# Optimization experiments

Hardware: AMD Instinct MI355X
Metric: run time of the kernel (lower is better)

Reference implementation:

```python
import jax, jax.numpy as jnp
import numpy as np

DETECTIONS_PER_IMG = 36
NMS_THRESH = 0.5
SCORE_THRESH = 0.2
MIN_SIZE = 0.01
NMS_TOPK = 2048  # fixed candidate budget for jit-compatible NMS
BBOX_XFORM_CLIP = float(np.log(1000.0 / 16.0))
WX, WY, WW, WH = 10.0, 10.0, 5.0, 5.0  # torchvision BoxCoder weights


def _decode(reg, props):
    # reg: [N, C*4], props: [N, 4] -> decoded boxes [N, C, 4] (torchvision BoxCoder.decode)
    widths = props[:, 2] - props[:, 0]
    heights = props[:, 3] - props[:, 1]
    ctr_x = props[:, 0] + 0.5 * widths
    ctr_y = props[:, 1] + 0.5 * heights
    reg = reg.reshape(reg.shape[0], -1, 4)
    dx = reg[..., 0] / WX
    dy = reg[..., 1] / WY
    dw = jnp.minimum(reg[..., 2] / WW, BBOX_XFORM_CLIP)
    dh = jnp.minimum(reg[..., 3] / WH, BBOX_XFORM_CLIP)
    pcx = dx * widths[:, None] + ctr_x[:, None]
    pcy = dy * heights[:, None] + ctr_y[:, None]
    pw = jnp.exp(dw) * widths[:, None]
    ph = jnp.exp(dh) * heights[:, None]
    return jnp.stack([pcx - 0.5 * pw, pcy - 0.5 * ph,
                      pcx + 0.5 * pw, pcy + 0.5 * ph], axis=-1)


def _pairwise_iou(boxes):
    # boxes: [K, 4] -> IoU [K, K]
    area = (boxes[:, 2] - boxes[:, 0]) * (boxes[:, 3] - boxes[:, 1])
    lt = jnp.maximum(boxes[:, None, :2], boxes[None, :, :2])
    rb = jnp.minimum(boxes[:, None, 2:], boxes[None, :, 2:])
    wh = jnp.clip(rb - lt, 0.0)
    inter = wh[..., 0] * wh[..., 1]
    union = area[:, None] + area[None, :] - inter
    return jnp.where(union > 0, inter / union, 0.0)


def _per_image(logits, reg, props, feats, img_hw):
    # logits [N, C], reg [N, C*4], props [N, 4], feats [N, D], img_hw [2] (h, w)
    N, C = logits.shape
    boxes = _decode(reg, props)[:, 1:, :].reshape(-1, 4)     # drop background, [N*(C-1), 4]
    scores = jax.nn.softmax(logits, axis=-1)[:, 1:].reshape(-1)
    h = img_hw[0].astype(boxes.dtype)
    w = img_hw[1].astype(boxes.dtype)
    x1 = jnp.clip(boxes[:, 0], 0.0, w)
    y1 = jnp.clip(boxes[:, 1], 0.0, h)
    x2 = jnp.clip(boxes[:, 2], 0.0, w)
    y2 = jnp.clip(boxes[:, 3], 0.0, h)
    boxes = jnp.stack([x1, y1, x2, y2], axis=-1)
    # score threshold + remove_small_boxes as a validity mask
    valid = (scores > SCORE_THRESH) & ((x2 - x1) >= MIN_SIZE) & ((y2 - y1) >= MIN_SIZE)
    masked = jnp.where(valid, scores, -jnp.inf)
    top_s, top_i = jax.lax.top_k(masked, NMS_TOPK)          # candidates in score order
    tboxes = boxes[top_i]
    tvalid = jnp.isfinite(top_s)
    iou = _pairwise_iou(tboxes)                              # [K, K]
    ar = jnp.arange(NMS_TOPK)

    def body(i, keep):
        sup = keep[i] & (iou[i] > NMS_THRESH) & (ar > i)
        return keep & ~sup

    keep = jax.lax.fori_loop(0, NMS_TOPK, body, tvalid)
    # first DETECTIONS_PER_IMG kept candidates, in score order (stable sort: kept first)
    order = jnp.argsort(jnp.where(keep, 0, 1), stable=True)[:DETECTIONS_PER_IMG]
    sel_keep = keep[order]
    prop_idx = top_i[order] // (C - 1)                       # candidate -> proposal row
    out = feats[prop_idx] * sel_keep[:, None].astype(feats.dtype)  # zero-pad missing slots
    return out


def setup_inputs() -> dict:
    key = jax.random.key(0)
    k0, k1, k2, k3, k4 = jax.random.split(key, 5)
    B, N, C, D = 8, 1000, 91, 1024
    class_logits = jax.random.normal(k0, (B, N, C), dtype=jnp.float32) * 3.0
    box_regression = jax.random.normal(k1, (B, N, C * 4), dtype=jnp.float32) * 0.5
    xy = jax.random.uniform(k2, (B, N, 2), minval=0.0, maxval=700.0)
    wh = jax.random.uniform(k3, (B, N, 2), minval=20.0, maxval=100.0)
    proposals = jnp.concatenate([xy, xy + wh], axis=-1).astype(jnp.float32)
    box_features = jax.random.normal(k4, (B, N, D), dtype=jnp.float32)
    image_shapes = jnp.full((B, 2), 800, dtype=jnp.int32)
    return {"class_logits": class_logits, "box_regression": box_regression,
            "proposals": proposals, "box_features": box_features,
            "image_shapes": image_shapes}


def reference(class_logits, box_regression, proposals, box_features, image_shapes):
    # returns [B, DETECTIONS_PER_IMG, D]
    return jax.vmap(_per_image)(class_logits, box_regression, proposals,
                                box_features, image_shapes)
```

## Files before the change

### kernel.cpp

```cpp
#include <hip/hip_runtime.h>
#include <stdint.h>

#define B 8
#define N 1000
#define C 91
#define NC 90
#define D 1024
#define KMAX 2048
#define PAD 4096
#define DETS 36
#define SCORE_THRESH 0.2f
#define NMS_THRESH 0.5f
#define MIN_SIZE 0.01f
#define XFORM_CLIP 4.135166556742356f

__device__ __forceinline__ void decode_clip(const float* __restrict__ rg,
                                            float wdt, float hgt, float cx, float cy,
                                            float W, float H,
                                            float& x1, float& y1, float& x2, float& y2) {
    float dx = rg[0] / 10.0f;
    float dy = rg[1] / 10.0f;
    float dw = fminf(rg[2] / 5.0f, XFORM_CLIP);
    float dh = fminf(rg[3] / 5.0f, XFORM_CLIP);
    float pcx = dx * wdt + cx;
    float pcy = dy * hgt + cy;
    float pw  = expf(dw) * wdt;
    float ph  = expf(dh) * hgt;
    x1 = fminf(fmaxf(pcx - 0.5f * pw, 0.0f), W);
    y1 = fminf(fmaxf(pcy - 0.5f * ph, 0.0f), H);
    x2 = fminf(fmaxf(pcx + 0.5f * pw, 0.0f), W);
    y2 = fminf(fmaxf(pcy + 0.5f * ph, 0.0f), H);
}

__global__ __launch_bounds__(256) void k_score(const float* __restrict__ logits,
                        const float* __restrict__ reg,
                        const float* __restrict__ props,
                        const int* __restrict__ img_hw,
                        unsigned long long* __restrict__ keys) {
    int b = blockIdx.x / 250;
    int local = blockIdx.x % 250;
    int wib = threadIdx.x >> 6, lane = threadIdx.x & 63;
    int n = local * 4 + wib;
    int r = b * N + n;

    __shared__ unsigned long long slot[4][4];
    if (threadIdx.x < 16) slot[threadIdx.x >> 2][threadIdx.x & 3] = 0ULL;
    __syncthreads();

    const float* lg = logits + (size_t)r * C;
    float v0 = lg[lane];
    float v1 = (lane < C - 64) ? lg[64 + lane] : -3.4e38f;
    float m = fmaxf(v0, v1);
    #pragma unroll
    for (int off = 32; off; off >>= 1) m = fmaxf(m, __shfl_xor(m, off, 64));
    float e0 = expf(v0 - m);
    float e1 = (lane < C - 64) ? expf(v1 - m) : 0.0f;
    float s = e0 + e1;
    #pragma unroll
    for (int off = 32; off; off >>= 1) s += __shfl_xor(s, off, 64);

    float p0 = props[r * 4 + 0], p1 = props[r * 4 + 1];
    float p2 = props[r * 4 + 2], p3 = props[r * 4 + 3];
    float wdt = p2 - p0, hgt = p3 - p1;
    float cx = p0 + 0.5f * wdt, cy = p1 + 0.5f * hgt;
    float H = (float)img_hw[b * 2 + 0];
    float W = (float)img_hw[b * 2 + 1];

    unsigned long long keyv[2] = {0ULL, 0ULL};
    #pragma unroll
    for (int t2 = 0; t2 < 2; ++t2) {
        int c = lane + t2 * 64;
        float e = t2 ? e1 : e0;
        if (c >= 1 && c < C) {
            float sc = e / s;
            if (sc > SCORE_THRESH) {
                const float* rg = reg + (size_t)r * (C * 4) + (size_t)c * 4;
                float x1, y1, x2, y2;
                decode_clip(rg, wdt, hgt, cx, cy, W, H, x1, y1, x2, y2);
                if ((x2 - x1) >= MIN_SIZE && (y2 - y1) >= MIN_SIZE) {
                    unsigned int idx = (unsigned int)(n * NC + (c - 1));
                    keyv[t2] = ((unsigned long long)__float_as_uint(sc) << 32) |
                               (unsigned long long)(0xFFFFFFFFu - idx);
                }
            }
        }
    }
    unsigned long long m0 = __ballot(keyv[0] != 0ULL);
    unsigned long long m1 = __ballot(keyv[1] != 0ULL);
    unsigned long long lower = (1ULL << lane) - 1ULL;
    if (keyv[0]) slot[wib][__popcll(m0 & lower)] = keyv[0];
    if (keyv[1]) slot[wib][__popcll(m0) + __popcll(m1 & lower)] = keyv[1];
    __syncthreads();
    if (threadIdx.x < 16) {
        int ww = threadIdx.x >> 2, p = threadIdx.x & 3;
        keys[(size_t)b * PAD + (size_t)(local * 4 + ww) * 4 + p] = slot[ww][p];
    }
}

__global__ __launch_bounds__(256) void k_rank(int* __restrict__ Kvals,
                                              const unsigned long long* __restrict__ keys,
                                              const float* __restrict__ reg,
                                              const float* __restrict__ props,
                                              const int* __restrict__ img_hw,
                                              float* __restrict__ bx1, float* __restrict__ by1,
                                              float* __restrict__ bx2, float* __restrict__ by2,
                                              int* __restrict__ propn) {
    __shared__ unsigned long long sk[PAD];
    __shared__ int pc[256];
    int b = blockIdx.y;
    const unsigned long long* kb = keys + (size_t)b * PAD;
    for (int t = threadIdx.x; t < PAD; t += 256)
        sk[t] = (t < 4 * N) ? kb[t] : 0ULL;
    __syncthreads();

    int rloc = threadIdx.x & 63;
    int quarter = threadIdx.x >> 6;
    int row = blockIdx.x * 64 + rloc;
    unsigned long long my = sk[row];
    int base = quarter * 1024;
    int cnt = 0;
    #pragma unroll 8
    for (int it = 0; it < 1024; ++it)
        cnt += (sk[base + it] > my) ? 1 : 0;
    pc[threadIdx.x] = cnt;
    __syncthreads();

    if (quarter == 0) {
        int rank = pc[rloc] + pc[rloc + 64] + pc[rloc + 128] + pc[rloc + 192];
        if (row == 4 * N) Kvals[b] = (rank < KMAX) ? rank : KMAX;
        if (my != 0ULL && rank < KMAX) {
            unsigned int idx = 0xFFFFFFFFu - (unsigned int)(my & 0xFFFFFFFFull);
            int n = (int)(idx / NC);
            int c = (int)(idx % NC) + 1;
            int r = b * N + n;
            float p0 = props[r * 4 + 0], p1 = props[r * 4 + 1];
            float p2 = props[r * 4 + 2], p3 = props[r * 4 + 3];
            float wdt = p2 - p0, hgt = p3 - p1;
            float cx = p0 + 0.5f * wdt, cy = p1 + 0.5f * hgt;
            float H = (float)img_hw[b * 2 + 0];
            float W = (float)img_hw[b * 2 + 1];
            const float* rg = reg + (size_t)r * (C * 4) + (size_t)c * 4;
            float x1, y1, x2, y2;
            decode_clip(rg, wdt, hgt, cx, cy, W, H, x1, y1, x2, y2);
            size_t o = (size_t)b * KMAX + rank;
            bx1[o] = x1; by1[o] = y1; bx2[o] = x2; by2[o] = y2;
            propn[o] = n;
        }
    }
}

__global__ __launch_bounds__(64) void k_nms(const int* __restrict__ Kvals,
                                            const float* __restrict__ bx1, const float* __restrict__ by1,
                                            const float* __restrict__ bx2, const float* __restrict__ by2,
                                            const int* __restrict__ propn,
                                            int* __restrict__ sel) {
    __shared__ float kx1[DETS], ky1[DETS], kx2[DETS], ky2[DETS];
    __shared__ int kpn[DETS];
    int b = blockIdx.x, lane = threadIdx.x;
    int K = Kvals[b];
    size_t ofs = (size_t)b * KMAX;
    int kept = 0;

    for (int cs = 0; cs < K && kept < DETS; cs += 64) {
        int j = cs + lane;
        bool inr = (j < K);
        int jj = inr ? j : 0;
        float x1 = bx1[ofs + jj], y1 = by1[ofs + jj];
        float x2 = bx2[ofs + jj], y2 = by2[ofs + jj];
        int pn = propn[ofs + jj];
        float area = (x2 - x1) * (y2 - y1);

        bool supp = !inr;
        for (int k = 0; k < kept; ++k) {
            float c1 = kx1[k], c2 = ky1[k], c3 = kx2[k], c4 = ky2[k];
            float carea = (c3 - c1) * (c4 - c2);
            float ix1 = fmaxf(c1, x1), iy1 = fmaxf(c2, y1);
            float ix2 = fminf(c3, x2), iy2 = fminf(c4, y2);
            float iw = fmaxf(ix2 - ix1, 0.0f), ih = fmaxf(iy2 - iy1, 0.0f);
            float inter = iw * ih;
            float uni = carea + area - inter;
            float iou = (uni > 0.0f) ? (inter / uni) : 0.0f;
            supp = supp || (iou > NMS_THRESH);
        }
        unsigned long long live = __ballot(!supp);
        while (live != 0ULL && kept < DETS) {
            int i = __ffsll((unsigned long long)live) - 1;
            float c1 = __shfl(x1, i, 64), c2 = __shfl(y1, i, 64);
            float c3 = __shfl(x2, i, 64), c4 = __shfl(y2, i, 64);
            int   cp = __shfl(pn, i, 64);
            if (lane == 0) { kx1[kept] = c1; ky1[kept] = c2; kx2[kept] = c3; ky2[kept] = c4; kpn[kept] = cp; }
            kept++;
            float carea = (c3 - c1) * (c4 - c2);
            float ix1 = fmaxf(c1, x1), iy1 = fmaxf(c2, y1);
            float ix2 = fminf(c3, x2), iy2 = fminf(c4, y2);
            float iw = fmaxf(ix2 - ix1, 0.0f), ih = fmaxf(iy2 - iy1, 0.0f);
            float inter = iw * ih;
            float uni = carea + area - inter;
            float iou = (uni > 0.0f) ? (inter / uni) : 0.0f;
            live &= ~__ballot(iou > NMS_THRESH);
        }
    }
    __syncthreads();
    if (lane < DETS) sel[b * DETS + lane] = (lane < kept) ? kpn[lane] : -1;
}

__global__ __launch_bounds__(256) void k_gather(const int* __restrict__ sel,
                                                const float* __restrict__ feats,
                                                float* __restrict__ out) {
    int slot = blockIdx.x;
    int b = slot / DETS;
    int row = sel[slot];
    float4* o = (float4*)(out + (size_t)slot * D);
    if (row >= 0) {
        const float4* f = (const float4*)(feats + ((size_t)b * N + row) * D);
        o[threadIdx.x] = f[threadIdx.x];
    } else {
        o[threadIdx.x] = make_float4(0.f, 0.f, 0.f, 0.f);
    }
}

extern "C" void kernel_launch(void* const* d_in, const int* in_sizes, int n_in,
                              void* d_out, int out_size, void* d_ws, size_t ws_size,
                              hipStream_t stream) {
    const float* logits = (const float*)d_in[0];
    const float* reg    = (const float*)d_in[1];
    const float* props  = (const float*)d_in[2];
    const float* feats  = (const float*)d_in[3];
    const int*   img    = (const int*)d_in[4];
    float* out = (float*)d_out;

    char* ws = (char*)d_ws;
    int* Kvals    = (int*)(ws + 0);
    int* sel      = (int*)(ws + 256);
    unsigned long long* keys = (unsigned long long*)(ws + 4096);
    float* bx1 = (float*)(ws + 270336);
    float* by1 = (float*)(ws + 335872);
    float* bx2 = (float*)(ws + 401408);
    float* by2 = (float*)(ws + 466944);
    int*   propn = (int*)(ws + 532480);

    k_score<<<dim3(B * 250), dim3(256), 0, stream>>>(logits, reg, props, img, keys);
    k_rank<<<dim3(64, B), dim3(256), 0, stream>>>(Kvals, keys,
        reg, props, img, bx1, by1, bx2, by2, propn);
    k_nms<<<dim3(B), dim3(64), 0, stream>>>(Kvals, bx1, by1, bx2, by2, propn, sel);
    k_gather<<<dim3(B * DETS), dim3(256), 0, stream>>>(sel, feats, out);
}
```

Measured before the change: 122.0 us.

## Register-block rank counting and fuse NMS with feature gather

Result: slower. 131.4 us (+7.7%).

```diff
diff --git a/kernel.cpp b/kernel.cpp
--- a/kernel.cpp
+++ b/kernel.cpp
@@ -97,7 +97,7 @@
     }
 }
 
-__global__ __launch_bounds__(256) void k_rank(int* __restrict__ Kvals,
+__global__ __launch_bounds__(512) void k_rank(int* __restrict__ Kvals,
                                               const unsigned long long* __restrict__ keys,
                                               const float* __restrict__ reg,
                                               const float* __restrict__ props,
@@ -106,27 +106,43 @@
                                               float* __restrict__ bx2, float* __restrict__ by2,
                                               int* __restrict__ propn) {
     __shared__ unsigned long long sk[PAD];
-    __shared__ int pc[256];
+    __shared__ int partial[8][256];
     int b = blockIdx.y;
     const unsigned long long* kb = keys + (size_t)b * PAD;
-    for (int t = threadIdx.x; t < PAD; t += 256)
+    for (int t = threadIdx.x; t < PAD; t += 512)
         sk[t] = (t < 4 * N) ? kb[t] : 0ULL;
     __syncthreads();
 
-    int rloc = threadIdx.x & 63;
-    int quarter = threadIdx.x >> 6;
-    int row = blockIdx.x * 64 + rloc;
-    unsigned long long my = sk[row];
-    int base = quarter * 1024;
-    int cnt = 0;
+    int w = threadIdx.x >> 6;
+    int lane = threadIdx.x & 63;
+    int rbase = blockIdx.x * 256;
+    unsigned long long my0 = sk[rbase + lane];
+    unsigned long long my1 = sk[rbase + lane + 64];
+    unsigned long long my2 = sk[rbase + lane + 128];
+    unsigned long long my3 = sk[rbase + lane + 192];
+    int c0 = 0, c1 = 0, c2 = 0, c3 = 0;
+    int base = w * 512;
     #pragma unroll 8
-    for (int it = 0; it < 1024; ++it)
-        cnt += (sk[base + it] > my) ? 1 : 0;
-    pc[threadIdx.x] = cnt;
-    __syncthreads();
-
-    if (quarter == 0) {
-        int rank = pc[rloc] + pc[rloc + 64] + pc[rloc + 128] + pc[rloc + 192];
+    for (int it = 0; it < 512; ++it) {
+        unsigned long long k = sk[base + it];
+        c0 += (k > my0) ? 1 : 0;
+        c1 += (k > my1) ? 1 : 0;
+        c2 += (k > my2) ? 1 : 0;
+        c3 += (k > my3) ? 1 : 0;
+    }
+    partial[w][lane]       = c0;
+    partial[w][lane + 64]  = c1;
+    partial[w][lane + 128] = c2;
+    partial[w][lane + 192] = c3;
+    __syncthreads();
+
+    if (threadIdx.x < 256) {
+        int rl = threadIdx.x;
+        int rank = 0;
+        #pragma unroll
+        for (int q = 0; q < 8; ++q) rank += partial[q][rl];
+        int row = rbase + rl;
+        unsigned long long my = sk[row];
         if (row == 4 * N) Kvals[b] = (rank < KMAX) ? rank : KMAX;
         if (my != 0ULL && rank < KMAX) {
             unsigned int idx = 0xFFFFFFFFu - (unsigned int)(my & 0xFFFFFFFFull);
@@ -149,73 +165,72 @@
     }
 }
 
-__global__ __launch_bounds__(64) void k_nms(const int* __restrict__ Kvals,
-                                            const float* __restrict__ bx1, const float* __restrict__ by1,
-                                            const float* __restrict__ bx2, const float* __restrict__ by2,
-                                            const int* __restrict__ propn,
-                                            int* __restrict__ sel) {
+__global__ __launch_bounds__(256) void k_nmsg(const int* __restrict__ Kvals,
+                                              const float* __restrict__ bx1, const float* __restrict__ by1,
+                                              const float* __restrict__ bx2, const float* __restrict__ by2,
+                                              const int* __restrict__ propn,
+                                              const float* __restrict__ feats,
+                                              float* __restrict__ out) {
     __shared__ float kx1[DETS], ky1[DETS], kx2[DETS], ky2[DETS];
     __shared__ int kpn[DETS];
+    __shared__ int skept;
     int b = blockIdx.x, lane = threadIdx.x;
-    int K = Kvals[b];
-    size_t ofs = (size_t)b * KMAX;
-    int kept = 0;
-
-    for (int cs = 0; cs < K && kept < DETS; cs += 64) {
-        int j = cs + lane;
-        bool inr = (j < K);
-        int jj = inr ? j : 0;
-        float x1 = bx1[ofs + jj], y1 = by1[ofs + jj];
-        float x2 = bx2[ofs + jj], y2 = by2[ofs + jj];
-        int pn = propn[ofs + jj];
-        float area = (x2 - x1) * (y2 - y1);
-
-        bool supp = !inr;
-        for (int k = 0; k < kept; ++k) {
-            float c1 = kx1[k], c2 = ky1[k], c3 = kx2[k], c4 = ky2[k];
-            float carea = (c3 - c1) * (c4 - c2);
-            float ix1 = fmaxf(c1, x1), iy1 = fmaxf(c2, y1);
-            float ix2 = fminf(c3, x2), iy2 = fminf(c4, y2);
-            float iw = fmaxf(ix2 - ix1, 0.0f), ih = fmaxf(iy2 - iy1, 0.0f);
-            float inter = iw * ih;
-            float uni = carea + area - inter;
-            float iou = (uni > 0.0f) ? (inter / uni) : 0.0f;
-            supp = supp || (iou > NMS_THRESH);
+
+    if (threadIdx.x < 64) {
+        int K = Kvals[b];
+        size_t ofs = (size_t)b * KMAX;
+        int kept = 0;
+        for (int cs = 0; cs < K && kept < DETS; cs += 64) {
+            int j = cs + lane;
+            bool inr = (j < K);
+            int jj = inr ? j : 0;
+            float x1 = bx1[ofs + jj], y1 = by1[ofs + jj];
+            float x2 = bx2[ofs + jj], y2 = by2[ofs + jj];
+            int pn = propn[ofs + jj];
+            float area = (x2 - x1) * (y2 - y1);
+
+            bool supp = !inr;
+            for (int k = 0; k < kept; ++k) {
+                float c1 = kx1[k], c2 = ky1[k], c3 = kx2[k], c4 = ky2[k];
+                float carea = (c3 - c1) * (c4 - c2);
+                float ix1 = fmaxf(c1, x1), iy1 = fmaxf(c2, y1);
+                float ix2 = fminf(c3, x2), iy2 = fminf(c4, y2);
+                float iw = fmaxf(ix2 - ix1, 0.0f), ih = fmaxf(iy2 - iy1, 0.0f);
+                float inter = iw * ih;
+                float uni = carea + area - inter;
+                float iou = (uni > 0.0f) ? (inter / uni) : 0.0f;
+                supp = supp || (iou > NMS_THRESH);
+            }
+            unsigned long long live = __ballot(!supp);
+            while (live != 0ULL && kept < DETS) {
+                int i = __ffsll((unsigned long long)live) - 1;
+                float c1 = __shfl(x1, i, 64), c2 = __shfl(y1, i, 64);
+                float c3 = __shfl(x2, i, 64), c4 = __shfl(y2, i, 64);
+                int   cp = __shfl(pn, i, 64);
+                if (lane == 0) { kx1[kept] = c1; ky1[kept] = c2; kx2[kept] = c3; ky2[kept] = c4; kpn[kept] = cp; }
+                kept++;
+                float carea = (c3 - c1) * (c4 - c2);
+                float ix1 = fmaxf(c1, x1), iy1 = fmaxf(c2, y1);
+                float ix2 = fminf(c3, x2), iy2 = fminf(c4, y2);
+                float iw = fmaxf(ix2 - ix1, 0.0f), ih = fmaxf(iy2 - iy1, 0.0f);
+                float inter = iw * ih;
+                float uni = carea + area - inter;
+                float iou = (uni > 0.0f) ? (inter / uni) : 0.0f;
+                live &= ~__ballot(iou > NMS_THRESH);
+            }
         }
-        unsigned long long live = __ballot(!supp);
-        while (live != 0ULL && kept < DETS) {
-            int i = __ffsll((unsigned long long)live) - 1;
-            float c1 = __shfl(x1, i, 64), c2 = __shfl(y1, i, 64);
-            float c3 = __shfl(x2, i, 64), c4 = __shfl(y2, i, 64);
-            int   cp = __shfl(pn, i, 64);
-            if (lane == 0) { kx1[kept] = c1; ky1[kept] = c2; kx2[kept] = c3; ky2[kept] = c4; kpn[kept] = cp; }
-            kept++;
-            float carea = (c3 - c1) * (c4 - c2);
-            float ix1 = fmaxf(c1, x1), iy1 = fmaxf(c2, y1);
-            float ix2 = fminf(c3, x2), iy2 = fminf(c4, y2);
-            float iw = fmaxf(ix2 - ix1, 0.0f), ih = fmaxf(iy2 - iy1, 0.0f);
-            float inter = iw * ih;
-            float uni = carea + area - inter;
-            float iou = (uni > 0.0f) ? (inter / uni) : 0.0f;
-            live &= ~__ballot(iou > NMS_THRESH);
-        }
-    }
-    __syncthreads();
-    if (lane < DETS) sel[b * DETS + lane] = (lane < kept) ? kpn[lane] : -1;
-}
-
-__global__ __launch_bounds__(256) void k_gather(const int* __restrict__ sel,
-                                                const float* __restrict__ feats,
-                                                float* __restrict__ out) {
-    int slot = blockIdx.x;
-    int b = slot / DETS;
-    int row = sel[slot];
-    float4* o = (float4*)(out + (size_t)slot * D);
-    if (row >= 0) {
-        const float4* f = (const float4*)(feats + ((size_t)b * N + row) * D);
-        o[threadIdx.x] = f[threadIdx.x];
-    } else {
-        o[threadIdx.x] = make_float4(0.f, 0.f, 0.f, 0.f);
+        if (lane == 0) skept = kept;
+    }
+    __syncthreads();
+
+    int kept = skept;
+    int t = threadIdx.x;
+    const float4* f4 = (const float4*)feats;
+    float4* o4 = (float4*)out;
+    for (int s = 0; s < DETS; ++s) {
+        float4 v = make_float4(0.f, 0.f, 0.f, 0.f);
+        if (s < kept) v = f4[((size_t)b * N + kpn[s]) * (D / 4) + t];
+        o4[((size_t)b * DETS + s) * (D / 4) + t] = v;
     }
 }
 
@@ -231,7 +246,6 @@
 
     char* ws = (char*)d_ws;
     int* Kvals    = (int*)(ws + 0);
-    int* sel      = (int*)(ws + 256);
     unsigned long long* keys = (unsigned long long*)(ws + 4096);
     float* bx1 = (float*)(ws + 270336);
     float* by1 = (float*)(ws + 335872);
@@ -240,8 +254,7 @@
     int*   propn = (int*)(ws + 532480);
 
     k_score<<<dim3(B * 250), dim3(256), 0, stream>>>(logits, reg, props, img, keys);
-    k_rank<<<dim3(64, B), dim3(256), 0, stream>>>(Kvals, keys,
+    k_rank<<<dim3(16, B), dim3(512), 0, stream>>>(Kvals, keys,
         reg, props, img, bx1, by1, bx2, by2, propn);
-    k_nms<<<dim3(B), dim3(64), 0, stream>>>(Kvals, bx1, by1, bx2, by2, propn, sel);
-    k_gather<<<dim3(B * DETS), dim3(256), 0, stream>>>(sel, feats, out);
-}
+    k_nmsg<<<dim3(B), dim3(256), 0, stream>>>(Kvals, bx1, by1, bx2, by2, propn, feats, out);
+}
```
